# Optimization experiments

Hardware: AMD Instinct MI355X
Metric: run time of the kernel (lower is better)

Reference implementation:

```python
import jax, jax.numpy as jnp
import numpy as np

N_NODES = 100000
N_EDGES = 3200000
IN_DIM = 256
HID = 64
OUT_DIM = 1


def gcn_conv(x, W, b, src, dst, n):
    # PyG GCNConv: h = x @ W; add self loops; sym-normalize; aggregate; + b
    h = x @ W  # [N, F]
    # degrees include self loops (edge_weight = 1), computed on target nodes
    ones = jnp.ones(src.shape[0], dtype=x.dtype)
    deg = jax.ops.segment_sum(ones, dst, num_segments=n) + 1.0  # +1 for self loop
    dinv = jax.lax.rsqrt(deg)
    norm = dinv[src] * dinv[dst]  # [E]
    msg = h[src] * norm[:, None]  # gather + scale
    out = jax.ops.segment_sum(msg, dst, num_segments=n)
    # self-loop contribution: norm_ii = dinv[i]^2
    out = out + h * (dinv * dinv)[:, None]
    return out + b


def setup_inputs() -> dict:
    key = jax.random.key(0)
    ks = jax.random.split(key, 6)
    x = jax.random.normal(ks[0], (N_NODES, IN_DIM), dtype=jnp.float32)
    edge_index = jax.random.randint(ks[1], (2, N_EDGES), 0, N_NODES, dtype=jnp.int64)
    W1 = jax.random.normal(ks[2], (IN_DIM, HID), dtype=jnp.float32) / np.sqrt(IN_DIM)
    b1 = jnp.zeros((HID,), dtype=jnp.float32)
    W2 = jax.random.normal(ks[3], (HID, HID), dtype=jnp.float32) / np.sqrt(HID)
    b2 = jnp.zeros((HID,), dtype=jnp.float32)
    Wf = jax.random.normal(ks[4], (HID, OUT_DIM), dtype=jnp.float32) / np.sqrt(HID)
    bf = jnp.zeros((OUT_DIM,), dtype=jnp.float32)
    return {"x": x, "edge_index": edge_index, "W1": W1, "b1": b1,
            "W2": W2, "b2": b2, "Wf": Wf, "bf": bf}


def reference(x, edge_index, W1, b1, W2, b2, Wf, bf):
    src, dst = edge_index[0], edge_index[1]
    n = x.shape[0]
    h = jax.nn.relu(gcn_conv(x, W1, b1, src, dst, n))
    h = jax.nn.relu(gcn_conv(h, W2, b2, src, dst, n))
    g = jnp.mean(h, axis=0)  # [HID] graph readout
    return jax.nn.sigmoid(g @ Wf + bf)  # [OUT_DIM]
```

## Files before the change

### kernel.cpp

```cpp
#include <hip/hip_runtime.h>


typedef unsigned int u32;
typedef unsigned short u16;
typedef unsigned char u8;
typedef short s16x8 __attribute__((ext_vector_type(8)));
typedef __bf16 bf16x8 __attribute__((ext_vector_type(8)));
typedef float f32x4 __attribute__((ext_vector_type(4)));

constexpr int HID  = 64;
constexpr int SH   = 7;
constexpr int BK   = 128;
constexpr int BPAD = 1024;
constexpr int CH   = 4096;
constexpr int SLOT = 5120;
constexpr int NBLK2 = 4096;

static __device__ __forceinline__ u8 f2fp8(float f) {
    int p = __builtin_amdgcn_cvt_pk_fp8_f32(f, f, 0, false);
    return (u8)(p & 0xFF);
}
static __device__ __forceinline__ float fp82f(u8 v) {
    return __builtin_amdgcn_cvt_f32_fp8((int)v, 0);
}
static __device__ __forceinline__ u16 f2bf(float f) {
    u32 u = __float_as_uint(f);
    return (u16)((u + 0x7FFFu + ((u >> 16) & 1u)) >> 16);
}

__global__ void pack_both_kernel(const float* __restrict__ W1, const float* __restrict__ W2,
                                 u16* __restrict__ wpack1, u16* __restrict__ wpack2) {
    int i = blockIdx.x * 256 + threadIdx.x;
    if (i < 256 * 64) {
        int e = i & 7, lane = (i >> 3) & 63, nt = (i >> 9) & 3, kk = i >> 11;
        wpack1[i] = f2bf(W1[(kk * 32 + (lane >> 4) * 8 + e) * HID + nt * 16 + (lane & 15)]);
    } else {
        int j = i - 256 * 64;
        if (j < 64 * 64) {
            int e = j & 7, lane = (j >> 3) & 63, nt = (j >> 9) & 3, kk = j >> 11;
            wpack2[j] = f2bf(W2[(kk * 32 + (lane >> 4) * 8 + e) * HID + nt * 16 + (lane & 15)]);
        }
    }
}

__global__ __launch_bounds__(256) void partition_kernel(const int* __restrict__ src,
                                                        const int* __restrict__ dst,
                                                        int* __restrict__ bcur,
                                                        u32* __restrict__ ep, int ne) {
    __shared__ int hcnt[BPAD];
    __shared__ int hoff[BPAD];
    __shared__ int gbase[BPAD];
    __shared__ u32 stage[CH];
    __shared__ int ssc[256];
    const int t = threadIdx.x;
    const int base = blockIdx.x * CH;
    const int cnt = min(CH, ne - base);
    for (int i = t; i < BPAD; i += 256) hcnt[i] = 0;
    __syncthreads();

    int myr[CH / 256];
    #pragma unroll
    for (int k = 0; k < CH / 256; ++k) {
        int i = t + k * 256;
        if (i < cnt) myr[k] = atomicAdd(&hcnt[dst[base + i] >> SH], 1);
    }
    __syncthreads();
    {
        int c0 = hcnt[t*4], c1 = hcnt[t*4+1], c2 = hcnt[t*4+2], c3 = hcnt[t*4+3];
        int tsum = c0 + c1 + c2 + c3;
        ssc[t] = tsum; __syncthreads();
        int run = tsum;
        for (int off = 1; off < 256; off <<= 1) {
            int v = (t >= off) ? ssc[t - off] : 0;
            __syncthreads();
            run += v; ssc[t] = run;
            __syncthreads();
        }
        int ex = run - tsum;
        hoff[t*4] = ex; ex += c0;
        hoff[t*4+1] = ex; ex += c1;
        hoff[t*4+2] = ex; ex += c2;
        hoff[t*4+3] = ex;
    }
    __syncthreads();
    for (int b = t; b < BPAD; b += 256) {
        int c = hcnt[b];
        if (c) gbase[b] = b * SLOT + atomicAdd(&bcur[b], c);
    }
    #pragma unroll
    for (int k = 0; k < CH / 256; ++k) {
        int i = t + k * 256;
        if (i < cnt) {
            int s = src[base + i], d = dst[base + i];
            stage[hoff[d >> SH] + myr[k]] = ((u32)(d & (BK - 1)) << 20) | (u32)s;
        }
    }
    __syncthreads();
    for (int i = t; i < cnt; i += 256) {
        u32 v = stage[i];
        int lo = 0;
        #pragma unroll
        for (int s = 512; s; s >>= 1) {
            int m = lo + s;
            if (m < BPAD && hoff[m] <= i) lo = m;
        }
        ep[gbase[lo] + (i - hoff[lo])] = v;
    }
}

__global__ __launch_bounds__(256) void sortgemm_kernel(const u32* __restrict__ ep,
                                                       const int* __restrict__ bcur,
                                                       int* __restrict__ eidx,
                                                       int* __restrict__ rowend,
                                                       float* __restrict__ dinv,
                                                       const float* __restrict__ x,
                                                       const u16* __restrict__ wpack1,
                                                       u8* __restrict__ hp, int n) {
    __shared__ int cnt[BK];
    __shared__ int sc[BK];
    __shared__ int cur[BK];
    __shared__ float sdv[BK];
    const int t = threadIdx.x, b = blockIdx.x;
    const int beg = b * SLOT, end = b * SLOT + bcur[b];
    if (t < BK) cnt[t] = 0;
    __syncthreads();
    for (int p = beg + t; p < end; p += 256) atomicAdd(&cnt[ep[p] >> 20], 1);
    __syncthreads();
    if (t < BK) sc[t] = cnt[t];
    __syncthreads();
    for (int o = 1; o < BK; o <<= 1) {
        int v = 0;
        if (t < BK && t >= o) v = sc[t - o];
        __syncthreads();
        if (t < BK) sc[t] += v;
        __syncthreads();
    }
    if (t < BK) {
        int node = b * BK + t;
        float dv = rsqrtf((float)cnt[t] + 1.0f);
        sdv[t] = dv;
        if (node < n) {
            rowend[node] = beg + sc[t];
            dinv[node] = dv;
        }
        cur[t] = beg + sc[t] - cnt[t];
    }
    __syncthreads();
    for (int p = beg + t; p < end; p += 256) {
        u32 v = ep[p];
        int r = atomicAdd(&cur[v >> 20], 1);
        eidx[r] = (int)(v & 0xFFFFFu);
    }
    __syncthreads();

    const int lane = t & 63;
    const int wid = t >> 6;
    const int r16 = lane & 15;
    const int kgrp = lane >> 4;
    #pragma unroll
    for (int it = 0; it < 2; ++it) {
        const int lrow0 = (wid * 2 + it) * 16;
        const int row0 = b * BK + lrow0;
        const int arow = row0 + r16;
        f32x4 acc[4] = {f32x4{0,0,0,0}, f32x4{0,0,0,0}, f32x4{0,0,0,0}, f32x4{0,0,0,0}};
        #pragma unroll
        for (int kk = 0; kk < 8; ++kk) {
            s16x8 abits;
            if (arow < n) {
                const float4* p0 = (const float4*)(x + (size_t)arow * 256 + kk * 32 + kgrp * 8);
                float4 v0 = p0[0], v1 = p0[1];
                abits[0] = (short)f2bf(v0.x); abits[1] = (short)f2bf(v0.y);
                abits[2] = (short)f2bf(v0.z); abits[3] = (short)f2bf(v0.w);
                abits[4] = (short)f2bf(v1.x); abits[5] = (short)f2bf(v1.y);
                abits[6] = (short)f2bf(v1.z); abits[7] = (short)f2bf(v1.w);
            } else {
                #pragma unroll
                for (int j = 0; j < 8; ++j) abits[j] = 0;
            }
            bf16x8 afrag = __builtin_bit_cast(bf16x8, abits);
            const u16* wp = wpack1 + ((size_t)(kk * 4) * 64 + lane) * 8;
            #pragma unroll
            for (int nt = 0; nt < 4; ++nt) {
                bf16x8 bfrag = *(const bf16x8*)(wp + (size_t)nt * 64 * 8);
                acc[nt] = __builtin_amdgcn_mfma_f32_16x16x32_bf16(afrag, bfrag, acc[nt], 0, 0, 0);
            }
        }
        #pragma unroll
        for (int reg = 0; reg < 4; ++reg) {
            int r = row0 + kgrp * 4 + reg;
            if (r < n) {
                float dv = sdv[lrow0 + kgrp * 4 + reg];
                #pragma unroll
                for (int nt = 0; nt < 4; ++nt)
                    hp[(size_t)r * HID + nt * 16 + r16] = f2fp8(acc[nt][reg] * dv);
            }
        }
    }
}

__global__ __launch_bounds__(256) void mfma_gemm2_kernel(const u8* __restrict__ A,
                                                         const u16* __restrict__ wpack,
                                                         const float* __restrict__ dinv,
                                                         u8* __restrict__ out8, int n) {
    const int t = threadIdx.x;
    const int lane = t & 63;
    const int wid = t >> 6;
    const int r16 = lane & 15;
    const int kgrp = lane >> 4;
    const int ntiles = (n + 15) >> 4;
    for (int tile = blockIdx.x * 4 + wid; tile < ntiles; tile += gridDim.x * 4) {
        const int row0 = tile * 16;
        const int arow = row0 + r16;
        f32x4 acc[4] = {f32x4{0,0,0,0}, f32x4{0,0,0,0}, f32x4{0,0,0,0}, f32x4{0,0,0,0}};
        #pragma unroll
        for (int kk = 0; kk < 2; ++kk) {
            s16x8 abits;
            u32 w0 = 0, w1 = 0;
            if (arow < n) {
                const u32* p0 = (const u32*)(A + (size_t)arow * 64 + kk * 32 + kgrp * 8);
                w0 = p0[0]; w1 = p0[1];
            }
            abits[0] = (short)f2bf(__builtin_amdgcn_cvt_f32_fp8((int)w0, 0));
            abits[1] = (short)f2bf(__builtin_amdgcn_cvt_f32_fp8((int)w0, 1));
            abits[2] = (short)f2bf(__builtin_amdgcn_cvt_f32_fp8((int)w0, 2));
            abits[3] = (short)f2bf(__builtin_amdgcn_cvt_f32_fp8((int)w0, 3));
            abits[4] = (short)f2bf(__builtin_amdgcn_cvt_f32_fp8((int)w1, 0));
            abits[5] = (short)f2bf(__builtin_amdgcn_cvt_f32_fp8((int)w1, 1));
            abits[6] = (short)f2bf(__builtin_amdgcn_cvt_f32_fp8((int)w1, 2));
            abits[7] = (short)f2bf(__builtin_amdgcn_cvt_f32_fp8((int)w1, 3));
            bf16x8 afrag = __builtin_bit_cast(bf16x8, abits);
            const u16* wp = wpack + ((size_t)(kk * 4) * 64 + lane) * 8;
            #pragma unroll
            for (int nt = 0; nt < 4; ++nt) {
                bf16x8 bfrag = *(const bf16x8*)(wp + (size_t)nt * 64 * 8);
                acc[nt] = __builtin_amdgcn_mfma_f32_16x16x32_bf16(afrag, bfrag, acc[nt], 0, 0, 0);
            }
        }
        #pragma unroll
        for (int reg = 0; reg < 4; ++reg) {
            int r = row0 + kgrp * 4 + reg;
            if (r < n) {
                float dv = dinv[r];
                #pragma unroll
                for (int nt = 0; nt < 4; ++nt)
                    out8[(size_t)r * HID + nt * 16 + r16] = f2fp8(acc[nt][reg] * dv);
            }
        }
    }
}

#define CVT4(acc0, acc1, acc2, acc3, wv) \
    acc0 += __builtin_amdgcn_cvt_f32_fp8((int)(wv), 0); \
    acc1 += __builtin_amdgcn_cvt_f32_fp8((int)(wv), 1); \
    acc2 += __builtin_amdgcn_cvt_f32_fp8((int)(wv), 2); \
    acc3 += __builtin_amdgcn_cvt_f32_fp8((int)(wv), 3);

__global__ __launch_bounds__(256) void agg_csr_kernel(const u8* __restrict__ hp,
                                                      const int* __restrict__ eidx,
                                                      const int* __restrict__ rowend,
                                                      const float* __restrict__ dinv,
                                                      const float* __restrict__ bias,
                                                      u8* __restrict__ out, int n) {
    int w = (blockIdx.x * 256 + threadIdx.x) >> 6;
    int lane = threadIdx.x & 63;
    if (w >= n) return;
    const int g = lane >> 4, fb = lane & 15;
    int beg = (w & (BK - 1)) ? rowend[w - 1] : (w >> SH) * SLOT;
    int end = rowend[w];
    float a0 = 0.f, a1 = 0.f, a2 = 0.f, a3 = 0.f;
    int p = beg;
    for (; p + 16 <= end; p += 16) {
        int s0 = __builtin_nontemporal_load(eidx + p + g);
        int s1 = __builtin_nontemporal_load(eidx + p + 4 + g);
        int s2 = __builtin_nontemporal_load(eidx + p + 8 + g);
        int s3 = __builtin_nontemporal_load(eidx + p + 12 + g);
        u32 w0 = *(const u32*)(hp + (size_t)s0 * 64 + fb * 4);
        u32 w1 = *(const u32*)(hp + (size_t)s1 * 64 + fb * 4);
        u32 w2 = *(const u32*)(hp + (size_t)s2 * 64 + fb * 4);
        u32 w3 = *(const u32*)(hp + (size_t)s3 * 64 + fb * 4);
        CVT4(a0, a1, a2, a3, w0)
        CVT4(a0, a1, a2, a3, w1)
        CVT4(a0, a1, a2, a3, w2)
        CVT4(a0, a1, a2, a3, w3)
    }
    for (; p < end; p += 4) {
        int idx = p + g;
        bool valid = idx < end;
        int s = __builtin_nontemporal_load(eidx + (valid ? idx : beg));
        u32 wv = *(const u32*)(hp + (size_t)s * 64 + fb * 4);
        if (valid) { CVT4(a0, a1, a2, a3, wv) }
    }
    a0 += __shfl_xor(a0, 16); a0 += __shfl_xor(a0, 32);
    a1 += __shfl_xor(a1, 16); a1 += __shfl_xor(a1, 32);
    a2 += __shfl_xor(a2, 16); a2 += __shfl_xor(a2, 32);
    a3 += __shfl_xor(a3, 16); a3 += __shfl_xor(a3, 32);
    u32 sv = *(const u32*)(hp + (size_t)w * 64 + fb * 4);
    float dv = dinv[w];
    float v0 = fmaxf(dv * (a0 + __builtin_amdgcn_cvt_f32_fp8((int)sv, 0)) + bias[fb * 4 + 0], 0.f);
    float v1 = fmaxf(dv * (a1 + __builtin_amdgcn_cvt_f32_fp8((int)sv, 1)) + bias[fb * 4 + 1], 0.f);
    float v2 = fmaxf(dv * (a2 + __builtin_amdgcn_cvt_f32_fp8((int)sv, 2)) + bias[fb * 4 + 2], 0.f);
    float v3 = fmaxf(dv * (a3 + __builtin_amdgcn_cvt_f32_fp8((int)sv, 3)) + bias[fb * 4 + 3], 0.f);
    if (g == 0) {
        int r = __builtin_amdgcn_cvt_pk_fp8_f32(v0, v1, 0, false);
        r = __builtin_amdgcn_cvt_pk_fp8_f32(v2, v3, r, true);
        *(u32*)(out + (size_t)w * 64 + fb * 4) = (u32)r;
    }
}

__global__ __launch_bounds__(256) void agg_csr_reduce_kernel(const u8* __restrict__ hp,
                                                             const int* __restrict__ eidx,
                                                             const int* __restrict__ rowend,
                                                             const float* __restrict__ dinv,
                                                             const float* __restrict__ bias,
                                                             float* __restrict__ partials, int n) {
    __shared__ float sred[256];
    int t = threadIdx.x, lane = t & 63;
    const int g = lane >> 4, fb = lane & 15;
    int wid = (blockIdx.x * 256 + t) >> 6;
    int wstride = gridDim.x * 4;
    float bl0 = bias[fb * 4 + 0], bl1 = bias[fb * 4 + 1];
    float bl2 = bias[fb * 4 + 2], bl3 = bias[fb * 4 + 3];
    float t0 = 0.f, t1 = 0.f, t2 = 0.f, t3 = 0.f;
    for (int w = wid; w < n; w += wstride) {
        int beg = (w & (BK - 1)) ? rowend[w - 1] : (w >> SH) * SLOT;
        int end = rowend[w];
        float a0 = 0.f, a1 = 0.f, a2 = 0.f, a3 = 0.f;
        int p = beg;
        for (; p + 16 <= end; p += 16) {
            int s0 = __builtin_nontemporal_load(eidx + p + g);
            int s1 = __builtin_nontemporal_load(eidx + p + 4 + g);
            int s2 = __builtin_nontemporal_load(eidx + p + 8 + g);
            int s3 = __builtin_nontemporal_load(eidx + p + 12 + g);
            u32 w0 = *(const u32*)(hp + (size_t)s0 * 64 + fb * 4);
            u32 w1 = *(const u32*)(hp + (size_t)s1 * 64 + fb * 4);
            u32 w2 = *(const u32*)(hp + (size_t)s2 * 64 + fb * 4);
            u32 w3 = *(const u32*)(hp + (size_t)s3 * 64 + fb * 4);
            CVT4(a0, a1, a2, a3, w0)
            CVT4(a0, a1, a2, a3, w1)
            CVT4(a0, a1, a2, a3, w2)
            CVT4(a0, a1, a2, a3, w3)
        }
        for (; p < end; p += 4) {
            int idx = p + g;
            bool valid = idx < end;
            int s = __builtin_nontemporal_load(eidx + (valid ? idx : beg));
            u32 wv = *(const u32*)(hp + (size_t)s * 64 + fb * 4);
            if (valid) { CVT4(a0, a1, a2, a3, wv) }
        }
        a0 += __shfl_xor(a0, 16); a0 += __shfl_xor(a0, 32);
        a1 += __shfl_xor(a1, 16); a1 += __shfl_xor(a1, 32);
        a2 += __shfl_xor(a2, 16); a2 += __shfl_xor(a2, 32);
        a3 += __shfl_xor(a3, 16); a3 += __shfl_xor(a3, 32);
        u32 sv = *(const u32*)(hp + (size_t)w * 64 + fb * 4);
        float dv = dinv[w];
        t0 += fmaxf(dv * (a0 + __builtin_amdgcn_cvt_f32_fp8((int)sv, 0)) + bl0, 0.f);
        t1 += fmaxf(dv * (a1 + __builtin_amdgcn_cvt_f32_fp8((int)sv, 1)) + bl1, 0.f);
        t2 += fmaxf(dv * (a2 + __builtin_amdgcn_cvt_f32_fp8((int)sv, 2)) + bl2, 0.f);
        t3 += fmaxf(dv * (a3 + __builtin_amdgcn_cvt_f32_fp8((int)sv, 3)) + bl3, 0.f);
    }
    int wv_ = t >> 6;
    if (g == 0) {
        sred[wv_ * 64 + fb * 4 + 0] = t0;
        sred[wv_ * 64 + fb * 4 + 1] = t1;
        sred[wv_ * 64 + fb * 4 + 2] = t2;
        sred[wv_ * 64 + fb * 4 + 3] = t3;
    }
    __syncthreads();
    if (t < 64) partials[blockIdx.x * 64 + t] = sred[t] + sred[t + 64] + sred[t + 128] + sred[t + 192];
}

__global__ __launch_bounds__(256) void gsum_stage_kernel(const float* __restrict__ parts, int nblk,
                                                         float* __restrict__ gsum) {
    __shared__ float sred[256];
    int t = threadIdx.x, col = t & 63;
    float a = 0.f;
    for (int bk = blockIdx.x * 4 + (t >> 6); bk < nblk; bk += gridDim.x * 4)
        a += parts[bk * 64 + col];
    sred[t] = a; __syncthreads();
    if (t < 64) atomicAdd(&gsum[t], sred[t] + sred[t + 64] + sred[t + 128] + sred[t + 192]);
}

__global__ void final_gsum_kernel(const float* __restrict__ gsum, const float* __restrict__ Wf,
                                  const float* __restrict__ bf_, float* __restrict__ out, float invn) {
    int lane = threadIdx.x;
    float v = gsum[lane] * invn * Wf[lane];
    #pragma unroll
    for (int off = 32; off; off >>= 1) v += __shfl_down(v, off);
    if (lane == 0) out[0] = 1.f / (1.f + expf(-(v + bf_[0])));
}

template <int K, typename TIn>
__global__ __launch_bounds__(256) void gemm_scale_kernel(const TIn* __restrict__ A,
                                                         const float* __restrict__ W,
                                                         const float* __restrict__ dinv,
                                                         u8* __restrict__ out8, int n) {
    __shared__ float xs[16][K];
    const int t = threadIdx.x;
    const int row0 = blockIdx.x * 16;
    if constexpr (sizeof(TIn) == 4) {
        const float* Af = (const float*)A;
        for (int i = t; i < 16 * K; i += 256) {
            int r = i / K;
            (&xs[0][0])[i] = (row0 + r < n) ? Af[(size_t)row0 * K + i] : 0.f;
        }
    } else {
        const u8* Ab = (const u8*)A;
        for (int i = t; i < 16 * K; i += 256) {
            int r = i / K;
            (&xs[0][0])[i] = (row0 + r < n) ? fp82f(Ab[(size_t)row0 * K + i]) : 0.f;
        }
    }
    __syncthreads();
    const int c = t & 63, rg = t >> 6;
    float acc[4] = {0.f, 0.f, 0.f, 0.f};
    #pragma unroll 4
    for (int k = 0; k < K; ++k) {
        float w = W[k * HID + c];
        #pragma unroll
        for (int j = 0; j < 4; ++j) acc[j] += xs[rg + 4 * j][k] * w;
    }
    #pragma unroll
    for (int j = 0; j < 4; ++j) {
        int r = row0 + rg + 4 * j;
        if (r < n) out8[(size_t)r * HID + c] = f2fp8(acc[j] * dinv[r]);
    }
}
__global__ void deg_f_kernel(const int* __restrict__ dst, float* __restrict__ deg, int ne) {
    int i = blockIdx.x * blockDim.x + threadIdx.x, st = gridDim.x * blockDim.x;
    for (; i < ne; i += st) atomicAdd(&deg[dst[i]], 1.0f);
}
__global__ void dinvf_kernel(float* __restrict__ deg, int n) {
    int i = blockIdx.x * blockDim.x + threadIdx.x;
    if (i < n) deg[i] = rsqrtf(deg[i] + 1.0f);
}
__global__ __launch_bounds__(256) void aggregate_atomic_kernel(const u8* __restrict__ hp,
        const int* __restrict__ src, const int* __restrict__ dst,
        const float* __restrict__ dinv, float* __restrict__ outf, int ne) {
    size_t tt = (size_t)blockIdx.x * 256 + threadIdx.x;
    int e = (int)(tt >> 6), f = (int)(tt & 63);
    if (e >= ne) return;
    int s = src[e], d = dst[e];
    atomicAdd(&outf[(size_t)d * HID + f], fp82f(hp[s * HID + f]) * dinv[d]);
}
__global__ void finalize1_fb_kernel(u8* __restrict__ hp, const float* __restrict__ agg,
                                    const float* __restrict__ dinv, const float* __restrict__ b, int n) {
    size_t i = (size_t)blockIdx.x * blockDim.x + threadIdx.x;
    if (i >= (size_t)n * HID) return;
    int node = (int)(i >> 6);
    float v = agg[i] + fp82f(hp[i]) * dinv[node] + b[i & 63];
    hp[i] = f2fp8(fmaxf(v, 0.f));
}
__global__ __launch_bounds__(256) void finalize2_fb_kernel(const u8* __restrict__ hp,
        const float* __restrict__ agg, const float* __restrict__ dinv,
        const float* __restrict__ b, float* __restrict__ gsum, int n) {
    __shared__ float sred[256];
    const int t = threadIdx.x, c = t & 63;
    const size_t total = (size_t)n * HID;
    const size_t stride = (size_t)gridDim.x * blockDim.x;
    float acc = 0.f;
    for (size_t i = (size_t)blockIdx.x * blockDim.x + t; i < total; i += stride) {
        int node = (int)(i >> 6);
        acc += fmaxf(agg[i] + fp82f(hp[i]) * dinv[node] + b[c], 0.f);
    }
    sred[t] = acc; __syncthreads();
    if (t < 64) atomicAdd(&gsum[c], sred[t] + sred[t + 64] + sred[t + 128] + sred[t + 192]);
}
__global__ void final_gsum_fb_kernel(const float* __restrict__ gsum, const float* __restrict__ Wf,
                                     const float* __restrict__ bf_, float* __restrict__ out, int n) {
    int lane = threadIdx.x;
    float v = (gsum[lane] / (float)n) * Wf[lane];
    #pragma unroll
    for (int off = 32; off; off >>= 1) v += __shfl_down(v, off);
    if (lane == 0) out[0] = 1.f / (1.f + expf(-(v + bf_[0])));
}

extern "C" void kernel_launch(void* const* d_in, const int* in_sizes, int n_in,
                              void* d_out, int out_size, void* d_ws, size_t ws_size,
                              hipStream_t stream) {
    const float* x  = (const float*)d_in[0];
    const int*   ei = (const int*)d_in[1];
    const float* W1 = (const float*)d_in[2];
    const float* b1 = (const float*)d_in[3];
    const float* W2 = (const float*)d_in[4];
    const float* b2 = (const float*)d_in[5];
    const float* Wf = (const float*)d_in[6];
    const float* bf_ = (const float*)d_in[7];
    float* out = (float*)d_out;

    const int n  = in_sizes[0] / 256;
    const int ne = in_sizes[1] / 2;
    const int* srcp = ei;
    const int* dstp = ei + ne;
    const int B = (n + BK - 1) / BK;

    char* p = (char*)d_ws;
    u32*   ep     = (u32*)p;   p += ((size_t)B * SLOT + 4096) * 4;
    int*   bcur   = (int*)p;   p += BPAD * 4;
    float* gsum   = (float*)p; p += 64 * 4;
    float* dinv   = (float*)p; p += (size_t)n * 4;
    int*   rowend = (int*)p;   p += (size_t)n * 4;
    int*   eidx   = (int*)p;   p += ((size_t)B * SLOT + 4096) * 4;
    float* parts  = (float*)p; p += (size_t)NBLK2 * 64 * 4;
    p = (char*)(((uintptr_t)p + 15) & ~(uintptr_t)15);
    u16*   wpack1 = (u16*)p;   p += 256 * 64 * 2;
    u16*   wpack2 = (u16*)p;   p += 64 * 64 * 2;
    u8*    hp     = (u8*)p;    p += (size_t)n * HID;
    u8*    h1     = (u8*)p;    p += (size_t)n * HID;
    size_t need = (size_t)(p - (char*)d_ws);

    bool slack_ok = ((size_t)ne / (size_t)B) <= (size_t)(SLOT - 1024);

    if (ws_size >= need && n <= (1 << 17) && slack_ok) {
        (void)hipMemsetAsync(bcur, 0, (BPAD + 64) * 4, stream);
        pack_both_kernel<<<80, 256, 0, stream>>>(W1, W2, wpack1, wpack2);

        const int PBLK = (ne + CH - 1) / CH;
        const int ntiles = (n + 15) / 16;
        const int GBLK = (ntiles + 3) / 4;
        partition_kernel<<<PBLK, 256, 0, stream>>>(srcp, dstp, bcur, ep, ne);
        sortgemm_kernel<<<B, 256, 0, stream>>>(ep, bcur, eidx, rowend, dinv, x, wpack1, hp, n);
        agg_csr_kernel<<<(n + 3) / 4, 256, 0, stream>>>(hp, eidx, rowend, dinv, b1, h1, n);
        mfma_gemm2_kernel<<<GBLK, 256, 0, stream>>>(h1, wpack2, dinv, hp, n);
        agg_csr_reduce_kernel<<<NBLK2, 256, 0, stream>>>(hp, eidx, rowend, dinv, b2, parts, n);
        gsum_stage_kernel<<<128, 256, 0, stream>>>(parts, NBLK2, gsum);
        final_gsum_kernel<<<1, 64, 0, stream>>>(gsum, Wf, bf_, out, 1.0f / (float)n);
    } else {
        char* q = (char*)d_ws;
        float* dinvF = (float*)q; q += (size_t)n * 4;
        float* gsumF = (float*)q; q += 64 * 4;
        u8*    hpF   = (u8*)q;   q += (size_t)n * HID;
        float* aggF  = (float*)q;

        (void)hipMemsetAsync(dinvF, 0, ((size_t)n + 64) * 4, stream);
        deg_f_kernel<<<2048, 256, 0, stream>>>(dstp, dinvF, ne);
        dinvf_kernel<<<(n + 255) / 256, 256, 0, stream>>>(dinvF, n);

        gemm_scale_kernel<256, float><<<(n + 15) / 16, 256, 0, stream>>>(x, W1, dinvF, hpF, n);
        (void)hipMemsetAsync(aggF, 0, (size_t)n * HID * 4, stream);
        aggregate_atomic_kernel<<<(int)(((size_t)ne * 64 + 255) / 256), 256, 0, stream>>>(hpF, srcp, dstp, dinvF, aggF, ne);
        finalize1_fb_kernel<<<(int)(((size_t)n * HID + 255) / 256), 256, 0, stream>>>(hpF, aggF, dinvF, b1, n);

        gemm_scale_kernel<64, u8><<<(n + 15) / 16, 256, 0, stream>>>(hpF, W2, dinvF, hpF, n);
        (void)hipMemsetAsync(aggF, 0, (size_t)n * HID * 4, stream);
        aggregate_atomic_kernel<<<(int)(((size_t)ne * 64 + 255) / 256), 256, 0, stream>>>(hpF, srcp, dstp, dinvF, aggF, ne);
        finalize2_fb_kernel<<<2048, 256, 0, stream>>>(hpF, aggF, dinvF, b2, gsumF, n);
        final_gsum_fb_kernel<<<1, 64, 0, stream>>>(gsumF, Wf, bf_, out, n);
    }
}
```

Before: 253.0 us.

## Split fused sort+GEMM1 into separate kernels, halve partition chunk, cache dst

```diff
diff --git a/kernel.cpp b/kernel.cpp
--- a/kernel.cpp
+++ b/kernel.cpp
@@ -12,7 +12,7 @@
 constexpr int SH   = 7;
 constexpr int BK   = 128;
 constexpr int BPAD = 1024;
-constexpr int CH   = 4096;
+constexpr int CH   = 2048;
 constexpr int SLOT = 5120;
 constexpr int NBLK2 = 4096;
 
@@ -59,10 +59,14 @@
     __syncthreads();
 
     int myr[CH / 256];
+    int myd[CH / 256];
     #pragma unroll
     for (int k = 0; k < CH / 256; ++k) {
         int i = t + k * 256;
-        if (i < cnt) myr[k] = atomicAdd(&hcnt[dst[base + i] >> SH], 1);
+        if (i < cnt) {
+            myd[k] = __builtin_nontemporal_load(dst + base + i);
+            myr[k] = atomicAdd(&hcnt[myd[k] >> SH], 1);
+        }
     }
     __syncthreads();
     {
@@ -91,7 +95,8 @@
     for (int k = 0; k < CH / 256; ++k) {
         int i = t + k * 256;
         if (i < cnt) {
-            int s = src[base + i], d = dst[base + i];
+            int s = __builtin_nontemporal_load(src + base + i);
+            int d = myd[k];
             stage[hoff[d >> SH] + myr[k]] = ((u32)(d & (BK - 1)) << 20) | (u32)s;
         }
     }
@@ -108,18 +113,14 @@
     }
 }
 
-__global__ __launch_bounds__(256) void sortgemm_kernel(const u32* __restrict__ ep,
-                                                       const int* __restrict__ bcur,
-                                                       int* __restrict__ eidx,
-                                                       int* __restrict__ rowend,
-                                                       float* __restrict__ dinv,
-                                                       const float* __restrict__ x,
-                                                       const u16* __restrict__ wpack1,
-                                                       u8* __restrict__ hp, int n) {
+__global__ __launch_bounds__(256) void bucket_sort_kernel(const u32* __restrict__ ep,
+                                                          const int* __restrict__ bcur,
+                                                          int* __restrict__ eidx,
+                                                          int* __restrict__ rowend,
+                                                          float* __restrict__ dinv, int n) {
     __shared__ int cnt[BK];
     __shared__ int sc[BK];
     __shared__ int cur[BK];
-    __shared__ float sdv[BK];
     const int t = threadIdx.x, b = blockIdx.x;
     const int beg = b * SLOT, end = b * SLOT + bcur[b];
     if (t < BK) cnt[t] = 0;
@@ -137,11 +138,9 @@
     }
     if (t < BK) {
         int node = b * BK + t;
-        float dv = rsqrtf((float)cnt[t] + 1.0f);
-        sdv[t] = dv;
         if (node < n) {
             rowend[node] = beg + sc[t];
-            dinv[node] = dv;
+            dinv[node] = rsqrtf((float)cnt[t] + 1.0f);
         }
         cur[t] = beg + sc[t] - cnt[t];
     }
@@ -151,28 +150,33 @@
         int r = atomicAdd(&cur[v >> 20], 1);
         eidx[r] = (int)(v & 0xFFFFFu);
     }
-    __syncthreads();
-
+}
+
+__global__ __launch_bounds__(256) void mfma_gemm1_kernel(const float* __restrict__ x,
+                                                         const u16* __restrict__ wpack1,
+                                                         const float* __restrict__ dinv,
+                                                         u8* __restrict__ hp, int n) {
+    const int t = threadIdx.x;
     const int lane = t & 63;
     const int wid = t >> 6;
     const int r16 = lane & 15;
     const int kgrp = lane >> 4;
-    #pragma unroll
-    for (int it = 0; it < 2; ++it) {
-        const int lrow0 = (wid * 2 + it) * 16;
-        const int row0 = b * BK + lrow0;
+    const int ntiles = (n + 15) >> 4;
+    for (int tile = blockIdx.x * 4 + wid; tile < ntiles; tile += gridDim.x * 4) {
+        const int row0 = tile * 16;
         const int arow = row0 + r16;
         f32x4 acc[4] = {f32x4{0,0,0,0}, f32x4{0,0,0,0}, f32x4{0,0,0,0}, f32x4{0,0,0,0}};
         #pragma unroll
         for (int kk = 0; kk < 8; ++kk) {
             s16x8 abits;
             if (arow < n) {
-                const float4* p0 = (const float4*)(x + (size_t)arow * 256 + kk * 32 + kgrp * 8);
-                float4 v0 = p0[0], v1 = p0[1];
-                abits[0] = (short)f2bf(v0.x); abits[1] = (short)f2bf(v0.y);
-                abits[2] = (short)f2bf(v0.z); abits[3] = (short)f2bf(v0.w);
-                abits[4] = (short)f2bf(v1.x); abits[5] = (short)f2bf(v1.y);
-                abits[6] = (short)f2bf(v1.z); abits[7] = (short)f2bf(v1.w);
+                const f32x4* p0 = (const f32x4*)(x + (size_t)arow * 256 + kk * 32 + kgrp * 8);
+                f32x4 v0 = __builtin_nontemporal_load(p0);
+                f32x4 v1 = __builtin_nontemporal_load(p0 + 1);
+                abits[0] = (short)f2bf(v0[0]); abits[1] = (short)f2bf(v0[1]);
+                abits[2] = (short)f2bf(v0[2]); abits[3] = (short)f2bf(v0[3]);
+                abits[4] = (short)f2bf(v1[0]); abits[5] = (short)f2bf(v1[1]);
+                abits[6] = (short)f2bf(v1[2]); abits[7] = (short)f2bf(v1[3]);
             } else {
                 #pragma unroll
                 for (int j = 0; j < 8; ++j) abits[j] = 0;
@@ -189,7 +193,7 @@
         for (int reg = 0; reg < 4; ++reg) {
             int r = row0 + kgrp * 4 + reg;
             if (r < n) {
-                float dv = sdv[lrow0 + kgrp * 4 + reg];
+                float dv = dinv[r];
                 #pragma unroll
                 for (int nt = 0; nt < 4; ++nt)
                     hp[(size_t)r * HID + nt * 16 + r16] = f2fp8(acc[nt][reg] * dv);
@@ -518,7 +522,8 @@
         const int ntiles = (n + 15) / 16;
         const int GBLK = (ntiles + 3) / 4;
         partition_kernel<<<PBLK, 256, 0, stream>>>(srcp, dstp, bcur, ep, ne);
-        sortgemm_kernel<<<B, 256, 0, stream>>>(ep, bcur, eidx, rowend, dinv, x, wpack1, hp, n);
+        bucket_sort_kernel<<<B, 256, 0, stream>>>(ep, bcur, eidx, rowend, dinv, n);
+        mfma_gemm1_kernel<<<GBLK, 256, 0, stream>>>(x, wpack1, dinv, hp, n);
         agg_csr_kernel<<<(n + 3) / 4, 256, 0, stream>>>(hp, eidx, rowend, dinv, b1, h1, n);
         mfma_gemm2_kernel<<<GBLK, 256, 0, stream>>>(h1, wpack2, dinv, hp, n);
         agg_csr_reduce_kernel<<<NBLK2, 256, 0, stream>>>(hp, eidx, rowend, dinv, b2, parts, n);
```

Result: slower. 292.0 us (+15.4%).
